# Kernel tuning notes

Hardware: AMD Instinct MI355X
Metric: run time of the kernel (lower is better)

Reference implementation:

```python
import jax, jax.numpy as jnp
import numpy as np

N, F, H, C = 8192, 512, 512, 64
SPARSITY = 0.5  # args.linear_sparsity


def _percentile(t, q):
    # torch kthvalue semantics: k = 1 + round(0.01*q*(n-1)), 1-indexed k-th smallest
    n = t.size
    k = int(1 + round(0.01 * q * (n - 1)))
    return jnp.sort(t.ravel())[k - 1]


def _pair_norm(x):
    x = x - x.mean(axis=0)
    rownorm_mean = jnp.sqrt(1e-6 + (x * x).sum(axis=1).mean())
    return x / rownorm_mean


def setup_inputs() -> dict:
    key = jax.random.key(0)
    ks = jax.random.split(key, 8)
    x = jax.random.normal(ks[0], (N, F), jnp.float32)
    adj = (jax.random.uniform(ks[1], (N, N)) < 0.002).astype(jnp.float32)
    W0 = jax.random.normal(ks[2], (H, F), jnp.float32) * (1.0 / np.sqrt(F))
    W1 = jax.random.normal(ks[3], (H, H), jnp.float32) * (1.0 / np.sqrt(H))
    W2 = jax.random.normal(ks[4], (C, H), jnp.float32) * (1.0 / np.sqrt(H))
    S0 = jax.random.normal(ks[5], (H, F), jnp.float32)
    S1 = jax.random.normal(ks[6], (H, H), jnp.float32)
    S2 = jax.random.normal(ks[7], (C, H), jnp.float32)
    return {"x": x, "adj": adj, "W0": W0, "W1": W1, "W2": W2,
            "S0": S0, "S1": S1, "S2": S2}


def reference(x, adj, W0, W1, W2, S0, S1, S2):
    # add self loops
    idx = jnp.arange(N)
    adj = adj.at[idx, idx].set(1.0)
    # global threshold over all |score| params (enable_abs_comp=True)
    all_scores = jnp.concatenate([jnp.abs(S0).ravel(), jnp.abs(S1).ravel(), jnp.abs(S2).ravel()])
    thr = _percentile(all_scores, SPARSITY * 100.0)
    # symmetric normalization D^-1/2 A D^-1/2
    deg_inv_sqrt = jnp.maximum(adj.sum(axis=-1), 1.0) ** -0.5
    adj_n = deg_inv_sqrt[:, None] * adj * deg_inv_sqrt[None, :]

    def masked_linear(h, W, S):
        Wm = W * (jnp.abs(S) > thr).astype(W.dtype)
        return h @ Wm.T

    # layers 0..num_layers-2 applied back-to-back (as in the source loop)
    h = masked_linear(x, W0, S0)
    h = masked_linear(h, W1, S1)
    h = adj_n @ h            # aggregation: [N,N] @ [N,H]
    h = _pair_norm(h)
    h = jax.nn.relu(h)
    h = masked_linear(h, W2, S2)
    return adj_n @ h          # [N, C]
```

## Files before the change

kernel.cpp:

```cpp
#include <hip/hip_runtime.h>
#include <hip/hip_bf16.h>

#define NN 8192
#define FF 512
#define HH 512
#define CC 64
#define NS_TOTAL 557056
#define KSEL 278529u
#define MAXNBR 96
#define MASKB 2176
#define NBINS 2048

typedef short short8 __attribute__((ext_vector_type(8)));
typedef __bf16 bf16x8 __attribute__((ext_vector_type(8)));
typedef float f32x4 __attribute__((ext_vector_type(4)));

__device__ __constant__ int kShift[3] = {21, 10, 0};

__device__ inline unsigned short f2bf(float f) {
    unsigned u = __float_as_uint(f);
    u += 0x7fffu + ((u >> 16) & 1u);
    return (unsigned short)(u >> 16);
}
__device__ inline float bf2f(unsigned short h) {
    return __uint_as_float(((unsigned)h) << 16);
}

__device__ inline f32x4 mfma16x16x32(short8 a, short8 b, f32x4 c) {
    return __builtin_amdgcn_mfma_f32_16x16x32_bf16(
        __builtin_bit_cast(bf16x8, a), __builtin_bit_cast(bf16x8, b), c, 0, 0, 0);
}

__device__ inline void gload_lds16(const unsigned short* g, unsigned short* l) {
    __builtin_amdgcn_global_load_lds(
        (const __attribute__((address_space(1))) void*)g,
        (__attribute__((address_space(3))) void*)l,
        16, 0, 0);
}

__device__ void deg_row_body(const float* __restrict__ adj, int* __restrict__ nnz,
                             int* __restrict__ colsI, float* __restrict__ dis,
                             int row, int* dcnt) {
    const int t = threadIdx.x;
    if (t == 0) *dcnt = 0;
    __syncthreads();
    const float4* arow = (const float4*)(adj + (size_t)row * NN);
    int* cp = colsI + (size_t)row * MAXNBR;
    for (int c4 = t; c4 < NN / 4; c4 += 256) {
        float4 v = arow[c4];
        int base = c4 * 4;
        float vv[4] = {v.x, v.y, v.z, v.w};
#pragma unroll
        for (int kq = 0; kq < 4; ++kq) {
            int col = base + kq;
            if (vv[kq] != 0.f || col == row) {
                int s = atomicAdd(dcnt, 1);
                if (s < MAXNBR) cp[s] = col;
            }
        }
    }
    __syncthreads();
    if (t == 0) {
        int c = *dcnt;
        nnz[row] = (c < MAXNBR) ? c : MAXNBR;
        dis[row] = rsqrtf((float)c);
    }
}

__device__ void isel2048(const unsigned* __restrict__ hist, unsigned k,
                         unsigned& bin, unsigned& krem) {
    __shared__ unsigned sh[256];
    __shared__ unsigned res[2];
    const int t = threadIdx.x;
    __syncthreads();
    unsigned g[8], sseg = 0;
#pragma unroll
    for (int i = 0; i < 8; ++i) { g[i] = hist[t * 8 + i]; sseg += g[i]; }
    sh[t] = sseg;
    __syncthreads();
    unsigned pre = 0;
    for (int i = 0; i < t; ++i) pre += sh[i];
    if (pre < k && k <= pre + sseg) {
        unsigned cum = pre;
        int i = 0;
        while (i < 7 && cum + g[i] < k) { cum += g[i]; ++i; }
        res[0] = (unsigned)(t * 8 + i);
        res[1] = k - cum;
    }
    __syncthreads();
    bin = res[0]; krem = res[1];
}

__device__ void isel_chain(const unsigned* __restrict__ hists, int npass,
                           unsigned& prefix, unsigned& k) {
    prefix = 0; k = KSEL;
    for (int p = 0; p < npass; ++p) {
        unsigned bin, krem;
        isel2048(hists + p * NBINS, k, bin, krem);
        prefix |= bin << kShift[p];
        k = krem;
    }
}


__global__ __launch_bounds__(256) void hist11_kernel(const float* __restrict__ S0,
                                                     const float* __restrict__ S1,
                                                     const float* __restrict__ S2,
                                                     unsigned* __restrict__ hists, int pass,
                                                     const float* __restrict__ adj,
                                                     int* __restrict__ nnz, int* __restrict__ colsI,
                                                     float* __restrict__ dis, int degRow0) {
    __shared__ unsigned lh[NBINS];
    __shared__ int dcnt;
    if ((int)blockIdx.x >= 256) {
        deg_row_body(adj, nnz, colsI, dis, degRow0 + (int)blockIdx.x - 256, &dcnt);
        return;
    }
    unsigned prefix = 0, k;
    if (pass > 0) isel_chain(hists, pass, prefix, k);
    int shift = kShift[pass];
    unsigned pmask = pass ? (0xFFFFFFFFu << kShift[pass - 1]) : 0u;
    unsigned dmask = (pass == 2) ? 0x3FFu : 0x7FFu;
    __syncthreads();
    for (int i = threadIdx.x; i < NBINS; i += 256) lh[i] = 0;
    __syncthreads();
    for (int idx = blockIdx.x * 256 + threadIdx.x; idx < NS_TOTAL; idx += 65536) {
        float v = (idx < 262144) ? S0[idx] : (idx < 524288) ? S1[idx - 262144] : S2[idx - 524288];
        unsigned key = __float_as_uint(fabsf(v));
        if ((key & pmask) == prefix)
            atomicAdd(&lh[(key >> shift) & dmask], 1u);
    }
    __syncthreads();
    for (int i = threadIdx.x; i < NBINS; i += 256) {
        unsigned c = lh[i];
        if (c) atomicAdd(&hists[pass * NBINS + i], c);
    }
}


__global__ __launch_bounds__(256) void mask_split_fused(
        const float* __restrict__ W0, const float* __restrict__ W1,
        const float* __restrict__ W2, const float* __restrict__ S0,
        const float* __restrict__ S1, const float* __restrict__ S2,
        const unsigned* __restrict__ hists,
        unsigned short* __restrict__ W0h, unsigned short* __restrict__ W0l,
        unsigned short* __restrict__ W1h, unsigned short* __restrict__ W1l,
        unsigned short* __restrict__ W2h, unsigned short* __restrict__ W2l,
        const float* __restrict__ X,
        unsigned short* __restrict__ Xh, unsigned short* __restrict__ Xl) {
    if (blockIdx.x >= MASKB) {
        int i = (blockIdx.x - MASKB) * 256 + threadIdx.x;
        float4 v = ((const float4*)X)[i];
        float vv[4] = {v.x, v.y, v.z, v.w};
        ushort4 hi, lo;
        unsigned short* hp = (unsigned short*)&hi;
        unsigned short* lp = (unsigned short*)&lo;
#pragma unroll
        for (int j = 0; j < 4; ++j) {
            hp[j] = f2bf(vv[j]);
            lp[j] = f2bf(vv[j] - bf2f(hp[j]));
        }
        *(ushort4*)&Xh[(size_t)i * 4] = hi;
        *(ushort4*)&Xl[(size_t)i * 4] = lo;
        return;
    }
    unsigned prefix, k;
    isel_chain(hists, 3, prefix, k);
    float thr = __uint_as_float(prefix);
    int idx = blockIdx.x * 256 + threadIdx.x;
    const float* W; const float* S; unsigned short* Yh; unsigned short* Yl; int i;
    if (idx < 262144)      { W = W0; S = S0; Yh = W0h; Yl = W0l; i = idx; }
    else if (idx < 524288) { W = W1; S = S1; Yh = W1h; Yl = W1l; i = idx - 262144; }
    else                   { W = W2; S = S2; Yh = W2h; Yl = W2l; i = idx - 524288; }
    float v = (fabsf(S[i]) > thr) ? W[i] : 0.f;
    unsigned short hi = f2bf(v);
    Yh[i] = hi;
    Yl[i] = f2bf(v - bf2f(hi));
}


template<int BMt, int BNt, int WRITE_SPLIT>
__global__ __launch_bounds__(256) void gemm_hl(
        const unsigned short* __restrict__ Ah, const unsigned short* __restrict__ Al,
        const unsigned short* __restrict__ Bh, const unsigned short* __restrict__ Bl,
        float* __restrict__ Cf, unsigned short* __restrict__ Ch,
        unsigned short* __restrict__ Cl, int Nn, int gridN) {
    constexpr int BK = 32;
    constexpr int MF = BMt / 32, NF = BNt / 32;
    __shared__ __align__(16) unsigned short AhS[BMt * BK], AlS[BMt * BK];
    __shared__ __align__(16) unsigned short BhS[BNt * BK], BlS[BNt * BK];

    const int tid = threadIdx.x, lane = tid & 63, wid = tid >> 6;
    const int wr = wid >> 1, wc = wid & 1;
    const int bm = ((int)blockIdx.x / gridN) * BMt;
    const int bn = ((int)blockIdx.x % gridN) * BNt;
    const int r16 = lane & 15, kg = lane >> 4;
    const int srow = lane >> 2;
    const int scol = ((lane & 3) ^ ((srow >> 1) & 3)) * 8;
    constexpr int cA = BMt / 16, cB = BNt / 16, CPW = (2 * cA + 2 * cB) / 4;
    f32x4 acc[MF][NF] = {};
    const int ksw = (kg ^ ((r16 >> 1) & 3)) * 8;
    const unsigned short* pAh = &AhS[(wr * (BMt / 2) + r16) * BK + ksw];
    const unsigned short* pAl = &AlS[(wr * (BMt / 2) + r16) * BK + ksw];
    const unsigned short* pBh = &BhS[(wc * (BNt / 2) + r16) * BK + ksw];
    const unsigned short* pBl = &BlS[(wc * (BNt / 2) + r16) * BK + ksw];

    for (int k0 = 0; k0 < 512; k0 += BK) {
        __syncthreads();
#pragma unroll
        for (int i = 0; i < CPW; ++i) {
            int c = wid * CPW + i;
            const unsigned short* src; unsigned short* dst; int cc, r0;
            if (c < cA)               { src = Ah; dst = AhS; cc = c;               r0 = bm + cc * 16; }
            else if (c < 2 * cA)      { src = Al; dst = AlS; cc = c - cA;          r0 = bm + cc * 16; }
            else if (c < 2 * cA + cB) { src = Bh; dst = BhS; cc = c - 2 * cA;      r0 = bn + cc * 16; }
            else                      { src = Bl; dst = BlS; cc = c - 2 * cA - cB; r0 = bn + cc * 16; }
            gload_lds16(src + (size_t)(r0 + srow) * 512 + k0 + scol, dst + cc * 512);
        }
        __syncthreads();
        short8 bhf[NF], blf[NF];
#pragma unroll
        for (int n = 0; n < NF; ++n) {
            bhf[n] = *(const short8*)(pBh + n * 16 * BK);
            blf[n] = *(const short8*)(pBl + n * 16 * BK);
        }
#pragma unroll
        for (int m = 0; m < MF; ++m) {
            short8 ahf = *(const short8*)(pAh + m * 16 * BK);
            short8 alf = *(const short8*)(pAl + m * 16 * BK);
#pragma unroll
            for (int n = 0; n < NF; ++n) {
                acc[m][n] = mfma16x16x32(ahf, bhf[n], acc[m][n]);
                acc[m][n] = mfma16x16x32(ahf, blf[n], acc[m][n]);
                acc[m][n] = mfma16x16x32(alf, bhf[n], acc[m][n]);
            }
        }
    }
#pragma unroll
    for (int m = 0; m < MF; ++m) {
#pragma unroll
        for (int n = 0; n < NF; ++n) {
            int row0 = bm + wr * (BMt / 2) + m * 16 + kg * 4;
            int col  = bn + wc * (BNt / 2) + n * 16 + r16;
#pragma unroll
            for (int j = 0; j < 4; ++j) {
                float v = acc[m][n][j];
                if (WRITE_SPLIT) {
                    unsigned short hi = f2bf(v);
                    size_t base = (size_t)(row0 + j) * Nn + col;
                    Ch[base] = hi;
                    Cl[base] = f2bf(v - bf2f(hi));
                } else {
                    Cf[(size_t)(row0 + j) * Nn + col] = v;
                }
            }
        }
    }
}


__global__ __launch_bounds__(256) void gemm3_pn(
        const float* __restrict__ hAgg,
        const unsigned short* __restrict__ Bh, const unsigned short* __restrict__ Bl,
        const float* __restrict__ colsum, const float* __restrict__ stats,
        float* __restrict__ Cf) {
    constexpr int BMt = 32, BNt = 64, BK = 32;
    constexpr int NF = 2;
    __shared__ __align__(16) unsigned short AhS[BMt * BK], AlS[BMt * BK];
    __shared__ __align__(16) unsigned short BhS[BNt * BK], BlS[BNt * BK];
    __shared__ float red[4];
    __shared__ float sbc;

    const int tid = threadIdx.x, lane = tid & 63, wid = tid >> 6;
    const int wr = wid >> 1, wc = wid & 1;
    const int bm = (int)blockIdx.x * BMt;
    const int r16 = lane & 15, kg = lane >> 4;
    const int srow = lane >> 2;
    const int scol = ((lane & 3) ^ ((srow >> 1) & 3)) * 8;
    const float inv = 1.0f / (float)NN;

    {
        float c0 = colsum[tid], c1 = colsum[tid + 256];
        float sq = c0 * c0 + c1 * c1;
#pragma unroll
        for (int o = 32; o > 0; o >>= 1) sq += __shfl_down(sq, o);
        if ((tid & 63) == 0) red[tid >> 6] = sq;
        __syncthreads();
        if (tid == 0) {
            float msum = red[0] + red[1] + red[2] + red[3];
            sbc = 1.0f / sqrtf(1e-6f + (stats[0] - msum * inv) * inv);
        }
        __syncthreads();
    }
    const float s = sbc;

    const int ar = tid >> 3, ac = (tid & 7) * 4;
    const int aoff = ar * 64 + (((ac >> 3) ^ ((ar >> 1) & 3)) * 16) + (ac & 7) * 2;

    f32x4 acc[1][NF] = {};
    const int ksw = (kg ^ ((r16 >> 1) & 3)) * 8;
    const unsigned short* pAh = &AhS[(wr * 16 + r16) * BK + ksw];
    const unsigned short* pAl = &AlS[(wr * 16 + r16) * BK + ksw];
    const unsigned short* pBh = &BhS[(wc * 32 + r16) * BK + ksw];
    const unsigned short* pBl = &BlS[(wc * 32 + r16) * BK + ksw];

    for (int k0 = 0; k0 < 512; k0 += BK) {
        __syncthreads();
#pragma unroll
        for (int i = 0; i < 2; ++i) {
            int c = wid * 2 + i;
            const unsigned short* src = (c < 4) ? Bh : Bl;
            unsigned short* dst = (c < 4) ? BhS : BlS;
            int cc = c & 3;
            gload_lds16(src + (size_t)(cc * 16 + srow) * 512 + k0 + scol, dst + cc * 512);
        }
        {
            float4 av = *(const float4*)(hAgg + (size_t)(bm + ar) * HH + k0 + ac);
            float4 m4 = *(const float4*)(colsum + k0 + ac);
            float vv[4];
            vv[0] = fmaxf((av.x - m4.x * inv) * s, 0.f);
            vv[1] = fmaxf((av.y - m4.y * inv) * s, 0.f);
            vv[2] = fmaxf((av.z - m4.z * inv) * s, 0.f);
            vv[3] = fmaxf((av.w - m4.w * inv) * s, 0.f);
            ushort4 hi, lo;
            unsigned short* hp = (unsigned short*)&hi;
            unsigned short* lp = (unsigned short*)&lo;
#pragma unroll
            for (int j = 0; j < 4; ++j) {
                hp[j] = f2bf(vv[j]);
                lp[j] = f2bf(vv[j] - bf2f(hp[j]));
            }
            *(ushort4*)((char*)AhS + aoff) = hi;
            *(ushort4*)((char*)AlS + aoff) = lo;
        }
        __syncthreads();
        short8 bhf[NF], blf[NF];
#pragma unroll
        for (int n = 0; n < NF; ++n) {
            bhf[n] = *(const short8*)(pBh + n * 16 * BK);
            blf[n] = *(const short8*)(pBl + n * 16 * BK);
        }
        short8 ahf = *(const short8*)pAh;
        short8 alf = *(const short8*)pAl;
#pragma unroll
        for (int n = 0; n < NF; ++n) {
            acc[0][n] = mfma16x16x32(ahf, bhf[n], acc[0][n]);
            acc[0][n] = mfma16x16x32(ahf, blf[n], acc[0][n]);
            acc[0][n] = mfma16x16x32(alf, bhf[n], acc[0][n]);
        }
    }
#pragma unroll
    for (int n = 0; n < NF; ++n) {
        int row0 = bm + wr * 16 + kg * 4;
        int col  = wc * 32 + n * 16 + r16;
#pragma unroll
        for (int j = 0; j < 4; ++j)
            Cf[(size_t)(row0 + j) * CC + col] = acc[0][n][j];
    }
}


__global__ void spmm512(const int* __restrict__ nnz, const int* __restrict__ colsI,
                        const float* __restrict__ dis, const float* __restrict__ Hin,
                        float* __restrict__ Hout) {
    int row = blockIdx.x;
    int t = threadIdx.x;
    int cnt = nnz[row];
    const int* cp = colsI + (size_t)row * MAXNBR;
    float4 acc = make_float4(0.f, 0.f, 0.f, 0.f);
    for (int j = 0; j < cnt; ++j) {
        int c = cp[j];
        float wgt = dis[c];
        float4 v = *(const float4*)(Hin + (size_t)c * HH + t * 4);
        acc.x += wgt * v.x; acc.y += wgt * v.y; acc.z += wgt * v.z; acc.w += wgt * v.w;
    }
    float di = dis[row];
    acc.x *= di; acc.y *= di; acc.z *= di; acc.w *= di;
    *(float4*)(Hout + (size_t)row * HH + t * 4) = acc;
}

__global__ void spmm64(const int* __restrict__ nnz, const int* __restrict__ colsI,
                       const float* __restrict__ dis, const float* __restrict__ Hin,
                       float* __restrict__ Hout) {
    int row = blockIdx.x;
    int t = threadIdx.x;
    int cnt = nnz[row];
    const int* cp = colsI + (size_t)row * MAXNBR;
    float acc = 0.f;
    for (int j = 0; j < cnt; ++j) {
        int c = cp[j];
        acc += dis[c] * Hin[(size_t)c * CC + t];
    }
    Hout[(size_t)row * CC + t] = dis[row] * acc;
}


__global__ void colstats_kernel(const float* __restrict__ X, float* __restrict__ colsum,
                                float* __restrict__ stats) {
    int t = threadIdx.x;
    float s0 = 0.f, s1 = 0.f, sq = 0.f;
    for (int r = blockIdx.x; r < NN; r += 256) {
        const float* row = X + (size_t)r * HH;
        float a = row[t], b = row[t + 256];
        s0 += a; s1 += b;
        sq += a * a + b * b;
    }
    atomicAdd(&colsum[t], s0);
    atomicAdd(&colsum[t + 256], s1);
#pragma unroll
    for (int o = 32; o > 0; o >>= 1) sq += __shfl_down(sq, o);
    __shared__ float red[4];
    int wv = t >> 6, lane = t & 63;
    if (lane == 0) red[wv] = sq;
    __syncthreads();
    if (t == 0) atomicAdd(stats, red[0] + red[1] + red[2] + red[3]);
}


extern "C" void kernel_launch(void* const* d_in, const int* in_sizes, int n_in,
                              void* d_out, int out_size, void* d_ws, size_t ws_size,
                              hipStream_t stream) {
    const float* x   = (const float*)d_in[0];
    const float* adj = (const float*)d_in[1];
    const float* W0  = (const float*)d_in[2];
    const float* W1  = (const float*)d_in[3];
    const float* W2  = (const float*)d_in[4];
    const float* S0  = (const float*)d_in[5];
    const float* S1  = (const float*)d_in[6];
    const float* S2  = (const float*)d_in[7];
    float* out = (float*)d_out;

    char* w = (char*)d_ws;
    size_t off = 0;
    auto alloc = [&](size_t b) { size_t r = off; off = (off + b + 255) & ~(size_t)255; return r; };
    unsigned* hists = (unsigned*)(w + alloc(3 * NBINS * 4));
    float* colsum   = (float*)(w + alloc(HH * 4));
    float* stats    = (float*)(w + alloc(256));
    size_t zero_end = off;
    int* nnz   = (int*)(w + alloc(NN * 4));
    int* colsI = (int*)(w + alloc((size_t)NN * MAXNBR * 4));
    float* dis = (float*)(w + alloc(NN * 4));
    unsigned short* xh  = (unsigned short*)(w + alloc((size_t)NN * FF * 2));
    unsigned short* xl  = (unsigned short*)(w + alloc((size_t)NN * FF * 2));
    unsigned short* W0h = (unsigned short*)(w + alloc((size_t)HH * FF * 2));
    unsigned short* W0l = (unsigned short*)(w + alloc((size_t)HH * FF * 2));
    unsigned short* W1h = (unsigned short*)(w + alloc((size_t)HH * HH * 2));
    unsigned short* W1l = (unsigned short*)(w + alloc((size_t)HH * HH * 2));
    unsigned short* W2h = (unsigned short*)(w + alloc((size_t)CC * HH * 2));
    unsigned short* W2l = (unsigned short*)(w + alloc((size_t)CC * HH * 2));
    unsigned short* hAh = (unsigned short*)(w + alloc((size_t)NN * HH * 2));
    unsigned short* hAl = (unsigned short*)(w + alloc((size_t)NN * HH * 2));
    float* hB   = (float*)(w + alloc((size_t)NN * HH * 4));
    float* hAgg = (float*)(w + alloc((size_t)NN * HH * 4));
    float* h3   = (float*)(w + alloc((size_t)NN * CC * 4));
    (void)ws_size; (void)in_sizes; (void)n_in; (void)out_size;

    hipMemsetAsync(d_ws, 0, zero_end, stream);

    const int degPer[3] = {2731, 2731, 2730};
    int degBase = 0;
    for (int p = 0; p < 3; ++p) {
        hist11_kernel<<<256 + degPer[p], 256, 0, stream>>>(S0, S1, S2, hists, p,
                                                           adj, nnz, colsI, dis, degBase);
        degBase += degPer[p];
    }

    mask_split_fused<<<MASKB + NN * FF / 4 / 256, 256, 0, stream>>>(
        W0, W1, W2, S0, S1, S2, hists, W0h, W0l, W1h, W1l, W2h, W2l, x, xh, xl);

    gemm_hl<64, 128, 1><<<(NN / 64) * (HH / 128), 256, 0, stream>>>(
        xh, xl, W0h, W0l, nullptr, hAh, hAl, HH, HH / 128);
    gemm_hl<64, 128, 0><<<(NN / 64) * (HH / 128), 256, 0, stream>>>(
        hAh, hAl, W1h, W1l, hB, nullptr, nullptr, HH, HH / 128);

    spmm512<<<NN, 128, 0, stream>>>(nnz, colsI, dis, hB, hAgg);

    colstats_kernel<<<256, 256, 0, stream>>>(hAgg, colsum, stats);

    gemm3_pn<<<NN / 32, 256, 0, stream>>>(hAgg, W2h, W2l, colsum, stats, h3);
    spmm64<<<NN, 64, 0, stream>>>(nnz, colsI, dis, h3, out);
}
```

Before: 211.9 us.

## Fuse column-sum and squared-norm stats into SpMM via adjacency column weights

Removes the separate colstats pass over the aggregated matrix. Column sums are computed algebraically as a weighted sum of the pre-aggregation rows, using per-column weights (sum of normalized adjacency entries) accumulated atomically during the degree pass. The squared-norm total is reduced inside the SpMM blocks from their outputs. This avoids re-reading the aggregated 8192x512 matrix, at the cost of extra atomics in the degree pass, an extra read of the input matrix by 256 extra blocks, and per-row block atomics on stats.

```diff
diff --git a/kernel.cpp b/kernel.cpp
--- a/kernel.cpp
+++ b/kernel.cpp
@@ -40,7 +40,7 @@
 
 __device__ void deg_row_body(const float* __restrict__ adj, int* __restrict__ nnz,
                              int* __restrict__ colsI, float* __restrict__ dis,
-                             int row, int* dcnt) {
+                             float* __restrict__ uvec, int row, int* dcnt, float* dshare) {
     const int t = threadIdx.x;
     if (t == 0) *dcnt = 0;
     __syncthreads();
@@ -62,9 +62,17 @@
     __syncthreads();
     if (t == 0) {
         int c = *dcnt;
-        nnz[row] = (c < MAXNBR) ? c : MAXNBR;
-        dis[row] = rsqrtf((float)c);
-    }
+        int cl = (c < MAXNBR) ? c : MAXNBR;
+        nnz[row] = cl;
+        float d = rsqrtf((float)c);
+        dis[row] = d;
+        *dshare = d;
+        *dcnt = cl;
+    }
+    __syncthreads();
+    float dr = *dshare;
+    int cl = *dcnt;
+    if (t < cl) atomicAdd(&uvec[cp[t]], dr);
 }
 
 __device__ void isel2048(const unsigned* __restrict__ hist, unsigned k,
@@ -109,11 +117,14 @@
                                                      unsigned* __restrict__ hists, int pass,
                                                      const float* __restrict__ adj,
                                                      int* __restrict__ nnz, int* __restrict__ colsI,
-                                                     float* __restrict__ dis, int degRow0) {
+                                                     float* __restrict__ dis,
+                                                     float* __restrict__ uvec, int degRow0) {
     __shared__ unsigned lh[NBINS];
     __shared__ int dcnt;
+    __shared__ float dshare;
     if ((int)blockIdx.x >= 256) {
-        deg_row_body(adj, nnz, colsI, dis, degRow0 + (int)blockIdx.x - 256, &dcnt);
+        deg_row_body(adj, nnz, colsI, dis, uvec, degRow0 + (int)blockIdx.x - 256,
+                     &dcnt, &dshare);
         return;
     }
     unsigned prefix = 0, k;
@@ -360,11 +371,29 @@
 }
 
 
-__global__ void spmm512(const int* __restrict__ nnz, const int* __restrict__ colsI,
-                        const float* __restrict__ dis, const float* __restrict__ Hin,
-                        float* __restrict__ Hout) {
+__global__ void spmm512_fused(const int* __restrict__ nnz, const int* __restrict__ colsI,
+                              const float* __restrict__ dis, const float* __restrict__ uvec,
+                              const float* __restrict__ Hin, float* __restrict__ Hout,
+                              float* __restrict__ colsum, float* __restrict__ stats) {
+    int t = threadIdx.x;
+    if ((int)blockIdx.x >= NN) {
+        int cb = (int)blockIdx.x - NN;
+        float a0 = 0.f, a1 = 0.f, a2 = 0.f, a3 = 0.f;
+        for (int j = cb; j < NN; j += 256) {
+            float wj = dis[j] * uvec[j];
+            const float* row = Hin + (size_t)j * HH;
+            a0 += wj * row[t];
+            a1 += wj * row[t + 128];
+            a2 += wj * row[t + 256];
+            a3 += wj * row[t + 384];
+        }
+        atomicAdd(&colsum[t], a0);
+        atomicAdd(&colsum[t + 128], a1);
+        atomicAdd(&colsum[t + 256], a2);
+        atomicAdd(&colsum[t + 384], a3);
+        return;
+    }
     int row = blockIdx.x;
-    int t = threadIdx.x;
     int cnt = nnz[row];
     const int* cp = colsI + (size_t)row * MAXNBR;
     float4 acc = make_float4(0.f, 0.f, 0.f, 0.f);
@@ -377,6 +406,13 @@
     float di = dis[row];
     acc.x *= di; acc.y *= di; acc.z *= di; acc.w *= di;
     *(float4*)(Hout + (size_t)row * HH + t * 4) = acc;
+    float sq = acc.x * acc.x + acc.y * acc.y + acc.z * acc.z + acc.w * acc.w;
+#pragma unroll
+    for (int o = 32; o > 0; o >>= 1) sq += __shfl_down(sq, o);
+    __shared__ float red[2];
+    if ((t & 63) == 0) red[t >> 6] = sq;
+    __syncthreads();
+    if (t == 0) atomicAdd(stats, red[0] + red[1]);
 }
 
 __global__ void spmm64(const int* __restrict__ nnz, const int* __restrict__ colsI,
@@ -392,28 +428,6 @@
         acc += dis[c] * Hin[(size_t)c * CC + t];
     }
     Hout[(size_t)row * CC + t] = dis[row] * acc;
-}
-
-
-__global__ void colstats_kernel(const float* __restrict__ X, float* __restrict__ colsum,
-                                float* __restrict__ stats) {
-    int t = threadIdx.x;
-    float s0 = 0.f, s1 = 0.f, sq = 0.f;
-    for (int r = blockIdx.x; r < NN; r += 256) {
-        const float* row = X + (size_t)r * HH;
-        float a = row[t], b = row[t + 256];
-        s0 += a; s1 += b;
-        sq += a * a + b * b;
-    }
-    atomicAdd(&colsum[t], s0);
-    atomicAdd(&colsum[t + 256], s1);
-#pragma unroll
-    for (int o = 32; o > 0; o >>= 1) sq += __shfl_down(sq, o);
-    __shared__ float red[4];
-    int wv = t >> 6, lane = t & 63;
-    if (lane == 0) red[wv] = sq;
-    __syncthreads();
-    if (t == 0) atomicAdd(stats, red[0] + red[1] + red[2] + red[3]);
 }
 
 
@@ -436,6 +450,7 @@
     unsigned* hists = (unsigned*)(w + alloc(3 * NBINS * 4));
     float* colsum   = (float*)(w + alloc(HH * 4));
     float* stats    = (float*)(w + alloc(256));
+    float* uvec     = (float*)(w + alloc(NN * 4));
     size_t zero_end = off;
     int* nnz   = (int*)(w + alloc(NN * 4));
     int* colsI = (int*)(w + alloc((size_t)NN * MAXNBR * 4));
@@ -461,7 +476,7 @@
     int degBase = 0;
     for (int p = 0; p < 3; ++p) {
         hist11_kernel<<<256 + degPer[p], 256, 0, stream>>>(S0, S1, S2, hists, p,
-                                                           adj, nnz, colsI, dis, degBase);
+                                                           adj, nnz, colsI, dis, uvec, degBase);
         degBase += degPer[p];
     }
 
@@ -473,9 +488,8 @@
     gemm_hl<64, 128, 0><<<(NN / 64) * (HH / 128), 256, 0, stream>>>(
         hAh, hAl, W1h, W1l, hB, nullptr, nullptr, HH, HH / 128);
 
-    spmm512<<<NN, 128, 0, stream>>>(nnz, colsI, dis, hB, hAgg);
-
-    colstats_kernel<<<256, 256, 0, stream>>>(hAgg, colsum, stats);
+    spmm512_fused<<<NN + 256, 128, 0, stream>>>(nnz, colsI, dis, uvec, hB, hAgg,
+                                                colsum, stats);
 
     gemm3_pn<<<NN / 32, 256, 0, stream>>>(hAgg, W2h, W2l, colsum, stats, h3);
     spmm64<<<NN, 64, 0, stream>>>(nnz, colsI, dis, h3, out);
```

Measured after the change: 286.2 us. +35.1%, slower.
